# Kernel optimization log

Measured on AMD Instinct MI355X. Metric: run time of the kernel, lower is better.

## Reference

```python
import jax, jax.numpy as jnp
import numpy as np

N_NODES = 100000
N_EDGES = 1600000
N_GRAPH = 100
IN_DIM = 64
LATENT = 128
STEPS = 2
MLP_LAYERS = 2
OUT_GLOBALS = 1
EPS = 1e-5  # haiku LayerNorm default


def setup_inputs() -> dict:
    key = jax.random.key(0)
    ks = jax.random.split(key, 8)
    nodes = jax.random.normal(ks[0], (N_NODES, IN_DIM), jnp.float32)
    senders = jax.random.randint(ks[1], (N_EDGES,), 0, N_NODES, jnp.int32)
    receivers = jax.random.randint(ks[2], (N_EDGES,), 0, N_NODES, jnp.int32)
    # 100 graphs of 1000 nodes each: jnp.repeat(arange(n_graph), n_node)
    graph_ids = (jnp.arange(N_NODES) // (N_NODES // N_GRAPH)).astype(jnp.int32)
    embed_w = jax.random.normal(ks[3], (IN_DIM, LATENT), jnp.float32) / np.sqrt(IN_DIM).astype(np.float32)
    embed_b = jnp.zeros((LATENT,), jnp.float32)
    mlp_w = jax.random.normal(ks[4], (STEPS, MLP_LAYERS, LATENT, LATENT), jnp.float32) / np.sqrt(LATENT).astype(np.float32)
    mlp_b = jnp.zeros((STEPS, MLP_LAYERS, LATENT), jnp.float32)
    ln_scale = jnp.ones((STEPS, LATENT), jnp.float32)
    ln_offset = jnp.zeros((STEPS, LATENT), jnp.float32)
    dec_w = jax.random.normal(ks[5], (LATENT, OUT_GLOBALS), jnp.float32) / np.sqrt(LATENT).astype(np.float32)
    dec_b = jnp.zeros((OUT_GLOBALS,), jnp.float32)
    return dict(nodes=nodes, senders=senders, receivers=receivers, graph_ids=graph_ids,
                embed_w=embed_w, embed_b=embed_b, mlp_w=mlp_w, mlp_b=mlp_b,
                ln_scale=ln_scale, ln_offset=ln_offset, dec_w=dec_w, dec_b=dec_b)


def _layernorm(x, scale, offset):
    mu = jnp.mean(x, axis=-1, keepdims=True)
    var = jnp.var(x, axis=-1, keepdims=True)
    return (x - mu) * jax.lax.rsqrt(var + EPS) * scale + offset


def reference(nodes, senders, receivers, graph_ids, embed_w, embed_b,
              mlp_w, mlp_b, ln_scale, ln_offset, dec_w, dec_b):
    n = nodes.shape[0]
    # jraph.GraphConvolution(add_self_edges=True, symmetric_normalization=True)
    self_loop = jnp.arange(n, dtype=senders.dtype)
    conv_s = jnp.concatenate([senders, self_loop])
    conv_r = jnp.concatenate([receivers, self_loop])
    ones_e = jnp.ones(conv_s.shape[0], jnp.float32)
    inv_sqrt_sdeg = jax.lax.rsqrt(jnp.maximum(jax.ops.segment_sum(ones_e, conv_s, n), 1.0))
    inv_sqrt_rdeg = jax.lax.rsqrt(jnp.maximum(jax.ops.segment_sum(ones_e, conv_r, n), 1.0))

    # embedder: hk.Linear on nodes
    h = nodes @ embed_w + embed_b

    for s in range(STEPS):
        # update_node_fn: MLP (dropout_rate=0 -> identity dropout)
        x = h
        for l in range(MLP_LAYERS):
            x = jax.nn.relu(x @ mlp_w[s, l] + mlp_b[s, l])
        # symmetric-normalized segment_sum aggregation with self-edges
        x = x * inv_sqrt_sdeg[:, None]
        x = jax.ops.segment_sum(x[conv_s], conv_r, num_segments=n)  # [n, LATENT]
        x = x * inv_sqrt_rdeg[:, None]
        h = x + h  # skip connection (add_graphs_tuples)
        h = _layernorm(h, ln_scale[s], ln_offset[s])

    # segment_mean pooling over graphs
    counts = jnp.maximum(jax.ops.segment_sum(jnp.ones(n, jnp.float32), graph_ids, N_GRAPH), 1.0)
    pooled = jax.ops.segment_sum(h, graph_ids, num_segments=N_GRAPH) / counts[:, None]
    # decoder: hk.Linear on pooled globals
    return pooled @ dec_w + dec_b  # [N_GRAPH, OUT_GLOBALS]
```

## Files before the change

### kernel.cpp

```cpp
#include <hip/hip_runtime.h>
#include <hip/hip_bf16.h>


#define N_NODES 100000
#define N_EDGES 1600000
#define N_GRAPH 100
#define NPG     1000
#define LATENT  128

#define NPART   4
#define PSIZE   (N_NODES / NPART)
#define NSLICE  64
#define ESLICE  (N_EDGES / NSLICE)

#define SCAN_CHUNK 2048
#define SCAN_NB    ((N_NODES + SCAN_CHUNK - 1) / SCAN_CHUNK)

typedef __attribute__((ext_vector_type(8))) short short8;
typedef __attribute__((ext_vector_type(4))) float f32x4;

__device__ __forceinline__ unsigned short f2bf(float f) {
    union { float f; unsigned int u; } v; v.f = f;
    unsigned int r = v.u + 0x7fff + ((v.u >> 16) & 1);
    return (unsigned short)(r >> 16);
}
__device__ __forceinline__ float bf2f(unsigned short u) {
    union { unsigned int u; float f; } v; v.u = ((unsigned int)u) << 16;
    return v.f;
}
__device__ __forceinline__ unsigned int pk_fp8x4(float a, float b, float c, float d) {
    int v = 0;
    v = __builtin_amdgcn_cvt_pk_fp8_f32(a, b, v, false);
    v = __builtin_amdgcn_cvt_pk_fp8_f32(c, d, v, true);
    return (unsigned int)v;
}

__global__ __launch_bounds__(1024) void k_hist2(const int* __restrict__ senders,
                                                const int* __restrict__ receivers,
                                                unsigned short* __restrict__ ps16,
                                                unsigned short* __restrict__ pr16) {
    __shared__ unsigned int cs[PSIZE / 2];
    __shared__ unsigned int cr[PSIZE / 2];
    int rg = blockIdx.x & (NPART - 1), sl = blockIdx.x >> 2;
    int lo = rg * PSIZE;
    for (int i = threadIdx.x; i < PSIZE / 2; i += 1024) { cs[i] = 0; cr[i] = 0; }
    __syncthreads();
    int e0 = sl * ESLICE;
    for (int e = e0 + threadIdx.x; e < e0 + ESLICE; e += 1024) {
        int s = senders[e] - lo;
        if ((unsigned)s < PSIZE) atomicAdd(&cs[s >> 1], 1u << ((s & 1) * 16));
        int r = receivers[e] - lo;
        if ((unsigned)r < PSIZE) atomicAdd(&cr[r >> 1], 1u << ((r & 1) * 16));
    }
    __syncthreads();
    size_t base = (size_t)(rg * NSLICE + sl) * PSIZE;
    for (int i = threadIdx.x; i < PSIZE; i += 1024) {
        ps16[base + i] = (unsigned short)((cs[i >> 1] >> ((i & 1) * 16)) & 0xffff);
        pr16[base + i] = (unsigned short)((cr[i >> 1] >> ((i & 1) * 16)) & 0xffff);
    }
}

__global__ __launch_bounds__(256) void k_scan_slices(const unsigned short* __restrict__ ps16,
                                                     unsigned short* __restrict__ pr16,
                                                     int* __restrict__ deg_r,
                                                     float* __restrict__ inv_s,
                                                     float* __restrict__ inv_r,
                                                     int* __restrict__ blocksums) {
    int t = threadIdx.x;
    int n = blockIdx.x * 256 + t;
    int run = 0, ss = 0;
    if (n < N_NODES) {
        int rg = n / PSIZE, i = n - rg * PSIZE;
        size_t base = (size_t)rg * NSLICE * PSIZE + i;
#pragma unroll 4
        for (int sl = 0; sl < NSLICE; sl++) {
            size_t idx = base + (size_t)sl * PSIZE;
            int v = pr16[idx];
            pr16[idx] = (unsigned short)run;
            run += v;
            ss += ps16[idx];
        }
        deg_r[n] = run;
        inv_r[n] = rsqrtf((float)(run + 1));
        inv_s[n] = rsqrtf((float)(ss + 1));
    }
    __shared__ int wsum[4];
    int s = run;
#pragma unroll
    for (int off = 32; off > 0; off >>= 1) s += __shfl_down(s, off, 64);
    if ((t & 63) == 0) wsum[t >> 6] = s;
    __syncthreads();
    if (t == 0)
        atomicAdd(&blocksums[blockIdx.x >> 3], wsum[0] + wsum[1] + wsum[2] + wsum[3]);
}

__global__ __launch_bounds__(256) void k_scan_apply(const int* __restrict__ deg,
                                                    const int* __restrict__ blocksums,
                                                    int* __restrict__ row_start, int n) {
    __shared__ int boff_s;
    int b = blockIdx.x, t = threadIdx.x;
    if (t < 64) {
        int v = (t < b && t < SCAN_NB) ? blocksums[t] : 0;
#pragma unroll
        for (int off = 32; off > 0; off >>= 1) v += __shfl_down(v, off, 64);
        if (t == 0) boff_s = v;
    }
    int base = b * SCAN_CHUNK + t * 8;
    int v[8]; int tsum = 0;
#pragma unroll
    for (int j = 0; j < 8; j++) { int i = base + j; v[j] = (i < n) ? deg[i] : 0; tsum += v[j]; }
    __shared__ int wtot[4];
    int inc = tsum;
#pragma unroll
    for (int off = 1; off < 64; off <<= 1) {
        int u = __shfl_up(inc, off, 64);
        if ((t & 63) >= off) inc += u;
    }
    if ((t & 63) == 63) wtot[t >> 6] = inc;
    __syncthreads();
    int wbase = 0;
    for (int w = 0; w < (t >> 6); w++) wbase += wtot[w];
    int running = boff_s + wbase + (inc - tsum);
#pragma unroll
    for (int j = 0; j < 8; j++) {
        int i = base + j;
        if (i < n) {
            row_start[i] = running;
            running += v[j];
            if (i == n - 1) row_start[n] = running;
        }
    }
}

__global__ __launch_bounds__(1024) void k_fill2(const int* __restrict__ senders,
                                                const int* __restrict__ receivers,
                                                const unsigned short* __restrict__ pr16,
                                                const int* __restrict__ row_start,
                                                int* __restrict__ edge_src) {
    __shared__ int bs[PSIZE];
    int rg = blockIdx.x & (NPART - 1), sl = blockIdx.x >> 2;
    int lo = rg * PSIZE;
    const unsigned short* base = pr16 + (size_t)(rg * NSLICE + sl) * PSIZE;
    for (int i = threadIdx.x; i < PSIZE; i += 1024)
        bs[i] = row_start[lo + i] + (int)base[i];
    __syncthreads();
    int e0 = sl * ESLICE;
    for (int e = e0 + threadIdx.x; e < e0 + ESLICE; e += 1024) {
        int r = receivers[e] - lo;
        if ((unsigned)r < PSIZE) {
            int pos = atomicAdd(&bs[r], 1);
            edge_src[pos] = senders[e];
        }
    }
}

__global__ void k_wprep(const float* __restrict__ embed_w, const float* __restrict__ mlp_w,
                        unsigned short* __restrict__ hi, unsigned short* __restrict__ lo) {
    int t = blockIdx.x * 256 + threadIdx.x;
    if (t >= 8192 + 4 * 16384) return;
    const float* src; int local;
    if (t < 8192) { src = embed_w; local = t; }
    else { int m = t - 8192; src = mlp_w + (size_t)(m >> 14) * 16384; local = m & 16383; }
    int j = local & 7, lane = (local >> 3) & 63, tn = (local >> 9) & 7, kc = local >> 12;
    int k = kc * 32 + ((lane >> 4) << 3) + j;
    int n = tn * 16 + (lane & 15);
    float wv = src[k * 128 + n];
    unsigned short h = f2bf(wv);
    float rem = wv - bf2f(h);
    hi[t] = h; lo[t] = f2bf(rem);
}

__global__ __launch_bounds__(256) void k_embed_mlp(
    const float* __restrict__ A,
    const unsigned short* __restrict__ wehi, const unsigned short* __restrict__ welo,
    const float* __restrict__ eb,
    const unsigned short* __restrict__ w0hi, const unsigned short* __restrict__ w0lo,
    const unsigned short* __restrict__ w1hi, const unsigned short* __restrict__ w1lo,
    const float* __restrict__ b0, const float* __restrict__ b1,
    const float* __restrict__ inv_s,
    unsigned short* __restrict__ h16, unsigned char* __restrict__ x8, int M)
{
    __shared__ __align__(16) unsigned short t0[4][32][136];
    int t = threadIdx.x, w = t >> 6, L = t & 63;
    int m0 = blockIdx.x * 128 + w * 32;
    int lr = L & 15, lk = (L >> 4) * 8, lq = (L >> 4) * 4;

    float ebv[8], b0v[8], b1v[8];
#pragma unroll
    for (int tn = 0; tn < 8; tn++) {
        ebv[tn] = eb[tn * 16 + lr];
        b0v[tn] = b0[tn * 16 + lr];
        b1v[tn] = b1[tn * 16 + lr];
    }

    f32x4 acc[2][8];
#pragma unroll
    for (int bd = 0; bd < 2; bd++)
#pragma unroll
        for (int tn = 0; tn < 8; tn++) acc[bd][tn] = (f32x4){0.f, 0.f, 0.f, 0.f};
#pragma unroll
    for (int kc = 0; kc < 2; kc++) {
        short8 a[2];
#pragma unroll
        for (int bd = 0; bd < 2; bd++) {
            int grow = m0 + bd * 16 + lr; if (grow >= M) grow = M - 1;
            const float* rp = A + (size_t)grow * 64 + kc * 32 + lk;
            float4 v0 = *(const float4*)rp;
            float4 v1 = *(const float4*)(rp + 4);
            short8 pk;
            pk[0] = (short)f2bf(v0.x); pk[1] = (short)f2bf(v0.y);
            pk[2] = (short)f2bf(v0.z); pk[3] = (short)f2bf(v0.w);
            pk[4] = (short)f2bf(v1.x); pk[5] = (short)f2bf(v1.y);
            pk[6] = (short)f2bf(v1.z); pk[7] = (short)f2bf(v1.w);
            a[bd] = pk;
        }
#pragma unroll
        for (int tn = 0; tn < 8; tn++) {
            size_t fo = (size_t)(((kc * 8 + tn) * 64 + L)) * 8;
            short8 bh = *(const short8*)(wehi + fo);
            short8 bl = *(const short8*)(welo + fo);
#pragma unroll
            for (int bd = 0; bd < 2; bd++) {
                acc[bd][tn] = __builtin_amdgcn_mfma_f32_16x16x32_bf16(a[bd], bh, acc[bd][tn], 0, 0, 0);
                acc[bd][tn] = __builtin_amdgcn_mfma_f32_16x16x32_bf16(a[bd], bl, acc[bd][tn], 0, 0, 0);
            }
        }
    }
#pragma unroll
    for (int bd = 0; bd < 2; bd++)
#pragma unroll
        for (int tn = 0; tn < 8; tn++)
#pragma unroll
            for (int r = 0; r < 4; r++)
                t0[w][bd * 16 + lq + r][tn * 16 + lr] = f2bf(acc[bd][tn][r] + ebv[tn]);
#pragma unroll
    for (int q = 0; q < 8; q++) {
        int s = q * 64 + L;
        int row = s >> 4, c0 = (s & 15) * 8;
        int grow = m0 + row;
        if (grow < M)
            *(short8*)(h16 + (size_t)grow * 128 + c0) = *(const short8*)&t0[w][row][c0];
    }

#pragma unroll
    for (int bd = 0; bd < 2; bd++)
#pragma unroll
        for (int tn = 0; tn < 8; tn++) acc[bd][tn] = (f32x4){0.f, 0.f, 0.f, 0.f};
#pragma unroll
    for (int kc = 0; kc < 4; kc++) {
        short8 a[2];
#pragma unroll
        for (int bd = 0; bd < 2; bd++)
            a[bd] = *(const short8*)&t0[w][bd * 16 + lr][kc * 32 + lk];
#pragma unroll
        for (int tn = 0; tn < 8; tn++) {
            size_t fo = (size_t)(((kc * 8 + tn) * 64 + L)) * 8;
            short8 bh = *(const short8*)(w0hi + fo);
            short8 bl = *(const short8*)(w0lo + fo);
#pragma unroll
            for (int bd = 0; bd < 2; bd++) {
                acc[bd][tn] = __builtin_amdgcn_mfma_f32_16x16x32_bf16(a[bd], bh, acc[bd][tn], 0, 0, 0);
                acc[bd][tn] = __builtin_amdgcn_mfma_f32_16x16x32_bf16(a[bd], bl, acc[bd][tn], 0, 0, 0);
            }
        }
    }
#pragma unroll
    for (int bd = 0; bd < 2; bd++)
#pragma unroll
        for (int tn = 0; tn < 8; tn++)
#pragma unroll
            for (int r = 0; r < 4; r++)
                t0[w][bd * 16 + lq + r][tn * 16 + lr] = f2bf(fmaxf(acc[bd][tn][r] + b0v[tn], 0.f));

#pragma unroll
    for (int bd = 0; bd < 2; bd++)
#pragma unroll
        for (int tn = 0; tn < 8; tn++) acc[bd][tn] = (f32x4){0.f, 0.f, 0.f, 0.f};
#pragma unroll
    for (int kc = 0; kc < 4; kc++) {
        short8 a[2];
#pragma unroll
        for (int bd = 0; bd < 2; bd++)
            a[bd] = *(const short8*)&t0[w][bd * 16 + lr][kc * 32 + lk];
#pragma unroll
        for (int tn = 0; tn < 8; tn++) {
            size_t fo = (size_t)(((kc * 8 + tn) * 64 + L)) * 8;
            short8 bh = *(const short8*)(w1hi + fo);
            short8 bl = *(const short8*)(w1lo + fo);
#pragma unroll
            for (int bd = 0; bd < 2; bd++) {
                acc[bd][tn] = __builtin_amdgcn_mfma_f32_16x16x32_bf16(a[bd], bh, acc[bd][tn], 0, 0, 0);
                acc[bd][tn] = __builtin_amdgcn_mfma_f32_16x16x32_bf16(a[bd], bl, acc[bd][tn], 0, 0, 0);
            }
        }
    }
    float invs[2][4];
#pragma unroll
    for (int bd = 0; bd < 2; bd++)
#pragma unroll
        for (int r = 0; r < 4; r++) {
            int grow = m0 + bd * 16 + lq + r; if (grow >= M) grow = M - 1;
            invs[bd][r] = inv_s[grow];
        }
#pragma unroll
    for (int bd = 0; bd < 2; bd++)
#pragma unroll
        for (int tn = 0; tn < 8; tn++)
#pragma unroll
            for (int r = 0; r < 4; r++)
                t0[w][bd * 16 + lq + r][tn * 16 + lr] =
                    f2bf(fmaxf(acc[bd][tn][r] + b1v[tn], 0.f) * invs[bd][r]);
#pragma unroll
    for (int q = 0; q < 8; q++) {
        int s = q * 64 + L;
        int row = s >> 4, c0 = (s & 15) * 8;
        int grow = m0 + row;
        if (grow < M) {
            const unsigned short* sp = &t0[w][row][c0];
            uint2 v;
            v.x = pk_fp8x4(bf2f(sp[0]), bf2f(sp[1]), bf2f(sp[2]), bf2f(sp[3]));
            v.y = pk_fp8x4(bf2f(sp[4]), bf2f(sp[5]), bf2f(sp[6]), bf2f(sp[7]));
            *(uint2*)(x8 + (size_t)grow * 128 + c0) = v;
        }
    }
}

__global__ __launch_bounds__(256) void k_mlp(
    const unsigned short* __restrict__ A16, const unsigned short* __restrict__ w0hi,
    const unsigned short* __restrict__ w0lo, const unsigned short* __restrict__ w1hi,
    const unsigned short* __restrict__ w1lo, const float* __restrict__ b0,
    const float* __restrict__ b1, const float* __restrict__ inv_s,
    unsigned char* __restrict__ x8, int M)
{
    __shared__ __align__(16) unsigned short t1[4][32][136];
    int t = threadIdx.x, w = t >> 6, L = t & 63;
    int m0 = blockIdx.x * 128 + w * 32;
    int lr = L & 15, lk = (L >> 4) * 8, lq = (L >> 4) * 4;

    float b0v[8], b1v[8];
#pragma unroll
    for (int tn = 0; tn < 8; tn++) { b0v[tn] = b0[tn * 16 + lr]; b1v[tn] = b1[tn * 16 + lr]; }

    f32x4 acc[2][8];
#pragma unroll
    for (int bd = 0; bd < 2; bd++)
#pragma unroll
        for (int tn = 0; tn < 8; tn++) acc[bd][tn] = (f32x4){0.f, 0.f, 0.f, 0.f};

#pragma unroll
    for (int kc = 0; kc < 4; kc++) {
        short8 a[2];
#pragma unroll
        for (int bd = 0; bd < 2; bd++) {
            int grow = m0 + bd * 16 + lr; if (grow >= M) grow = M - 1;
            a[bd] = *(const short8*)(A16 + (size_t)grow * 128 + kc * 32 + lk);
        }
#pragma unroll
        for (int tn = 0; tn < 8; tn++) {
            size_t fo = (size_t)(((kc * 8 + tn) * 64 + L)) * 8;
            short8 bh = *(const short8*)(w0hi + fo);
            short8 bl = *(const short8*)(w0lo + fo);
#pragma unroll
            for (int bd = 0; bd < 2; bd++) {
                acc[bd][tn] = __builtin_amdgcn_mfma_f32_16x16x32_bf16(a[bd], bh, acc[bd][tn], 0, 0, 0);
                acc[bd][tn] = __builtin_amdgcn_mfma_f32_16x16x32_bf16(a[bd], bl, acc[bd][tn], 0, 0, 0);
            }
        }
    }
#pragma unroll
    for (int bd = 0; bd < 2; bd++)
#pragma unroll
        for (int tn = 0; tn < 8; tn++)
#pragma unroll
            for (int r = 0; r < 4; r++)
                t1[w][bd * 16 + lq + r][tn * 16 + lr] = f2bf(fmaxf(acc[bd][tn][r] + b0v[tn], 0.f));

    f32x4 acc2[2][8];
#pragma unroll
    for (int bd = 0; bd < 2; bd++)
#pragma unroll
        for (int tn = 0; tn < 8; tn++) acc2[bd][tn] = (f32x4){0.f, 0.f, 0.f, 0.f};
#pragma unroll
    for (int kc = 0; kc < 4; kc++) {
        short8 a[2];
#pragma unroll
        for (int bd = 0; bd < 2; bd++)
            a[bd] = *(const short8*)&t1[w][bd * 16 + lr][kc * 32 + lk];
#pragma unroll
        for (int tn = 0; tn < 8; tn++) {
            size_t fo = (size_t)(((kc * 8 + tn) * 64 + L)) * 8;
            short8 bh = *(const short8*)(w1hi + fo);
            short8 bl = *(const short8*)(w1lo + fo);
#pragma unroll
            for (int bd = 0; bd < 2; bd++) {
                acc2[bd][tn] = __builtin_amdgcn_mfma_f32_16x16x32_bf16(a[bd], bh, acc2[bd][tn], 0, 0, 0);
                acc2[bd][tn] = __builtin_amdgcn_mfma_f32_16x16x32_bf16(a[bd], bl, acc2[bd][tn], 0, 0, 0);
            }
        }
    }
    float invs[2][4];
#pragma unroll
    for (int bd = 0; bd < 2; bd++)
#pragma unroll
        for (int r = 0; r < 4; r++) {
            int grow = m0 + bd * 16 + lq + r; if (grow >= M) grow = M - 1;
            invs[bd][r] = inv_s[grow];
        }
#pragma unroll
    for (int bd = 0; bd < 2; bd++)
#pragma unroll
        for (int tn = 0; tn < 8; tn++)
#pragma unroll
            for (int r = 0; r < 4; r++)
                t1[w][bd * 16 + lq + r][tn * 16 + lr] =
                    f2bf(fmaxf(acc2[bd][tn][r] + b1v[tn], 0.f) * invs[bd][r]);
#pragma unroll
    for (int q = 0; q < 8; q++) {
        int s = q * 64 + L;
        int row = s >> 4, c0 = (s & 15) * 8;
        int grow = m0 + row;
        if (grow < M) {
            const unsigned short* sp = &t1[w][row][c0];
            uint2 v;
            v.x = pk_fp8x4(bf2f(sp[0]), bf2f(sp[1]), bf2f(sp[2]), bf2f(sp[3]));
            v.y = pk_fp8x4(bf2f(sp[4]), bf2f(sp[5]), bf2f(sp[6]), bf2f(sp[7]));
            *(uint2*)(x8 + (size_t)grow * 128 + c0) = v;
        }
    }
}

__device__ __forceinline__ float2 agg_gather8(const unsigned char* __restrict__ x8,
                                              const int* __restrict__ edge_src,
                                              int node, int L, int beg, int end)
{
    unsigned short su = *(const unsigned short*)(x8 + (size_t)node * 128 + 2 * L);
    float2 acc;
    acc.x = __builtin_amdgcn_cvt_f32_fp8((int)su, 0);
    acc.y = __builtin_amdgcn_cvt_f32_fp8((int)su, 1);

    int j = beg;
    for (; j + 8 <= end; j += 8) {
        unsigned short u[8];
#pragma unroll
        for (int q = 0; q < 8; q++)
            u[q] = *(const unsigned short*)(x8 + (size_t)edge_src[j + q] * 128 + 2 * L);
#pragma unroll
        for (int q = 0; q < 8; q++) {
            acc.x += __builtin_amdgcn_cvt_f32_fp8((int)u[q], 0);
            acc.y += __builtin_amdgcn_cvt_f32_fp8((int)u[q], 1);
        }
    }
    if (j < end) {
        int last = end - 1;
        unsigned short u[8];
#pragma unroll
        for (int q = 0; q < 8; q++) {
            int jj = j + q; if (jj > last) jj = last;
            u[q] = *(const unsigned short*)(x8 + (size_t)edge_src[jj] * 128 + 2 * L);
        }
#pragma unroll
        for (int q = 0; q < 8; q++) {
            float a = __builtin_amdgcn_cvt_f32_fp8((int)u[q], 0);
            float b = __builtin_amdgcn_cvt_f32_fp8((int)u[q], 1);
            if (j + q <= last) { acc.x += a; acc.y += b; }
        }
    }
    return acc;
}

__global__ __launch_bounds__(256) void k_agg_ln(
    const unsigned char* __restrict__ x8, const int* __restrict__ row_start,
    const int* __restrict__ edge_src, const float* __restrict__ inv_r,
    const float* __restrict__ ln_scale, const float* __restrict__ ln_offset,
    unsigned short* __restrict__ h16)
{
    int node = __builtin_amdgcn_readfirstlane(blockIdx.x * 4 + (threadIdx.x >> 6));
    int L = threadIdx.x & 63;
    const unsigned int* h32 = (const unsigned int*)h16;

    int beg = row_start[node], end = row_start[node + 1];
    float2 acc = agg_gather8(x8, edge_src, node, L, beg, end);

    float ir = inv_r[node];
    unsigned int hu = h32[(size_t)node * 64 + L];
    float y0 = acc.x * ir + __uint_as_float(hu << 16);
    float y1 = acc.y * ir + __uint_as_float(hu & 0xffff0000u);

    float s1 = y0 + y1, s2 = y0 * y0 + y1 * y1;
#pragma unroll
    for (int off = 32; off > 0; off >>= 1) {
        s1 += __shfl_xor(s1, off, 64);
        s2 += __shfl_xor(s2, off, 64);
    }
    float mu = s1 * (1.f / 128.f);
    float var = fmaxf(s2 * (1.f / 128.f) - mu * mu, 0.f);
    float rstd = rsqrtf(var + 1e-5f);
    float2 sc = *(const float2*)&ln_scale[L * 2];
    float2 of = *(const float2*)&ln_offset[L * 2];
    float ox = (y0 - mu) * rstd * sc.x + of.x;
    float oy = (y1 - mu) * rstd * sc.y + of.y;
    ((unsigned int*)h16)[(size_t)node * 64 + L] =
        (unsigned int)f2bf(ox) | ((unsigned int)f2bf(oy) << 16);
}

__global__ __launch_bounds__(256) void k_agg_pool(
    const unsigned char* __restrict__ x8, const int* __restrict__ row_start,
    const int* __restrict__ edge_src, const float* __restrict__ inv_r,
    const float* __restrict__ ln_scale, const float* __restrict__ ln_offset,
    const unsigned short* __restrict__ h16, float* __restrict__ poolpart)
{
    __shared__ float2 part[4][64];
    int w = threadIdx.x >> 6, L = threadIdx.x & 63;
    int node = __builtin_amdgcn_readfirstlane(blockIdx.x * 4 + w);
    const unsigned int* h32 = (const unsigned int*)h16;

    int beg = row_start[node], end = row_start[node + 1];
    float2 acc = agg_gather8(x8, edge_src, node, L, beg, end);

    float ir = inv_r[node];
    unsigned int hu = h32[(size_t)node * 64 + L];
    float y0 = acc.x * ir + __uint_as_float(hu << 16);
    float y1 = acc.y * ir + __uint_as_float(hu & 0xffff0000u);

    float s1 = y0 + y1, s2 = y0 * y0 + y1 * y1;
#pragma unroll
    for (int off = 32; off > 0; off >>= 1) {
        s1 += __shfl_xor(s1, off, 64);
        s2 += __shfl_xor(s2, off, 64);
    }
    float mu = s1 * (1.f / 128.f);
    float var = fmaxf(s2 * (1.f / 128.f) - mu * mu, 0.f);
    float rstd = rsqrtf(var + 1e-5f);
    float2 sc = *(const float2*)&ln_scale[L * 2];
    float2 of = *(const float2*)&ln_offset[L * 2];
    float2 o;
    o.x = (y0 - mu) * rstd * sc.x + of.x;
    o.y = (y1 - mu) * rstd * sc.y + of.y;
    part[w][L] = o;
    __syncthreads();
    if (w == 0) {
        float2 p0 = part[0][L], p1 = part[1][L], p2 = part[2][L], p3 = part[3][L];
        float2 s;
        s.x = (p0.x + p1.x) + (p2.x + p3.x);
        s.y = (p0.y + p1.y) + (p2.y + p3.y);
        *(float2*)&poolpart[(size_t)blockIdx.x * 128 + L * 2] = s;
    }
}

__global__ __launch_bounds__(128) void k_pool2(const float* __restrict__ poolpart,
                                               float* __restrict__ poolpart2) {
    int b = blockIdx.x, col = threadIdx.x;
    const float* pg = poolpart + ((size_t)b * 25) * 128;
    float s = 0.f;
#pragma unroll
    for (int k = 0; k < 25; k++) s += pg[k * 128 + col];
    poolpart2[(size_t)b * 128 + col] = s;
}

__global__ __launch_bounds__(128) void k_pool3(const float* __restrict__ poolpart2,
                                               const float* __restrict__ dec_w,
                                               const float* __restrict__ dec_b,
                                               float* __restrict__ out) {
    int g = blockIdx.x, col = threadIdx.x;
    const float* pg = poolpart2 + (size_t)g * 10 * 128;
    float s = 0.f;
#pragma unroll
    for (int c = 0; c < 10; c++) s += pg[c * 128 + col];
    s = s * (1.f / (float)NPG) * dec_w[col];
    __shared__ float ws[2];
#pragma unroll
    for (int off = 32; off > 0; off >>= 1) s += __shfl_down(s, off, 64);
    if ((col & 63) == 0) ws[col >> 6] = s;
    __syncthreads();
    if (col == 0) out[g] = ws[0] + ws[1] + dec_b[0];
}

extern "C" void kernel_launch(void* const* d_in, const int* in_sizes, int n_in,
                              void* d_out, int out_size, void* d_ws, size_t ws_size,
                              hipStream_t stream) {
    (void)in_sizes; (void)n_in; (void)out_size; (void)ws_size;
    const float* nodes     = (const float*)d_in[0];
    const int*   senders   = (const int*)d_in[1];
    const int*   receivers = (const int*)d_in[2];
    const float* embed_w   = (const float*)d_in[4];
    const float* embed_b   = (const float*)d_in[5];
    const float* mlp_w     = (const float*)d_in[6];
    const float* mlp_b     = (const float*)d_in[7];
    const float* ln_scale  = (const float*)d_in[8];
    const float* ln_offset = (const float*)d_in[9];
    const float* dec_w     = (const float*)d_in[10];
    const float* dec_b     = (const float*)d_in[11];
    float* out = (float*)d_out;

    const int N = N_NODES;
    const int WF_TOTAL = 8192 + 4 * 16384;
    const size_t PART_TOTAL = (size_t)NPART * NSLICE * PSIZE;

    char* p = (char*)d_ws;
    auto alloc = [&](size_t bytes) -> void* {
        void* r = (void*)p;
        p += (bytes + 255) & ~(size_t)255;
        return r;
    };
    unsigned short* h16      = (unsigned short*)alloc((size_t)N * 128 * 2);
    unsigned char*  x8       = (unsigned char*)alloc((size_t)N * 128);
    int*            edge_src = (int*)alloc((size_t)N_EDGES * 4);
    unsigned short* ps16     = (unsigned short*)alloc(PART_TOTAL * 2);
    unsigned short* pr16     = (unsigned short*)alloc(PART_TOTAL * 2);
    int*            deg_r    = (int*)alloc((size_t)N * 4);
    float*          inv_s    = (float*)alloc((size_t)N * 4);
    float*          inv_r    = (float*)alloc((size_t)N * 4);
    int*            row_start= (int*)alloc((size_t)(N + 1) * 4);
    int*            blocksums= (int*)alloc((size_t)SCAN_NB * 4);
    unsigned short* wfhi     = (unsigned short*)alloc((size_t)WF_TOTAL * 2);
    unsigned short* wflo     = (unsigned short*)alloc((size_t)WF_TOTAL * 2);
    float*          poolpart = (float*)alloc((size_t)(N / 4) * 128 * 4);
    float*          poolpart2= (float*)alloc((size_t)1000 * 128 * 4);

    hipMemsetAsync(blocksums, 0, (size_t)SCAN_NB * 4, stream);
    k_wprep<<<(WF_TOTAL + 255) / 256, 256, 0, stream>>>(embed_w, mlp_w, wfhi, wflo);

    k_hist2<<<NPART * NSLICE, 1024, 0, stream>>>(senders, receivers, ps16, pr16);
    k_scan_slices<<<(N + 255) / 256, 256, 0, stream>>>(ps16, pr16, deg_r, inv_s, inv_r, blocksums);
    k_scan_apply<<<SCAN_NB, 256, 0, stream>>>(deg_r, blocksums, row_start, N);
    k_fill2<<<NPART * NSLICE, 1024, 0, stream>>>(senders, receivers, pr16, row_start, edge_src);

    int mblocks = (N + 127) / 128;
    const unsigned short* wehi = wfhi, *welo = wflo;
    const unsigned short* w0hi[2] = { wfhi + 8192,             wfhi + 8192 + 2 * 16384 };
    const unsigned short* w0lo[2] = { wflo + 8192,             wflo + 8192 + 2 * 16384 };
    const unsigned short* w1hi[2] = { wfhi + 8192 + 16384,     wfhi + 8192 + 3 * 16384 };
    const unsigned short* w1lo[2] = { wflo + 8192 + 16384,     wflo + 8192 + 3 * 16384 };

    k_embed_mlp<<<mblocks, 256, 0, stream>>>(nodes, wehi, welo, embed_b,
                                             w0hi[0], w0lo[0], w1hi[0], w1lo[0],
                                             mlp_b, mlp_b + 128, inv_s, h16, x8, N);
    k_agg_ln<<<N / 4, 256, 0, stream>>>(x8, row_start, edge_src, inv_r,
                                        ln_scale, ln_offset, h16);
    k_mlp<<<mblocks, 256, 0, stream>>>(h16, w0hi[1], w0lo[1], w1hi[1], w1lo[1],
                                       mlp_b + 256, mlp_b + 384, inv_s, x8, N);
    k_agg_pool<<<N / 4, 256, 0, stream>>>(x8, row_start, edge_src, inv_r,
                                          ln_scale + 128, ln_offset + 128, h16, poolpart);

    k_pool2<<<1000, 128, 0, stream>>>(poolpart, poolpart2);
    k_pool3<<<N_GRAPH, 128, 0, stream>>>(poolpart2, dec_w, dec_b, out);
}
```

Baseline: 355.2 us.

## Record per-edge rank in histogram pass and fill CSR without atomics

Measured after the change: 366.7 us. +3.2%, slower.

```diff
diff --git a/kernel.cpp b/kernel.cpp
--- a/kernel.cpp
+++ b/kernel.cpp
@@ -38,7 +38,8 @@
 __global__ __launch_bounds__(1024) void k_hist2(const int* __restrict__ senders,
                                                 const int* __restrict__ receivers,
                                                 unsigned short* __restrict__ ps16,
-                                                unsigned short* __restrict__ pr16) {
+                                                unsigned short* __restrict__ pr16,
+                                                unsigned short* __restrict__ rank) {
     __shared__ unsigned int cs[PSIZE / 2];
     __shared__ unsigned int cr[PSIZE / 2];
     int rg = blockIdx.x & (NPART - 1), sl = blockIdx.x >> 2;
@@ -50,7 +51,10 @@
         int s = senders[e] - lo;
         if ((unsigned)s < PSIZE) atomicAdd(&cs[s >> 1], 1u << ((s & 1) * 16));
         int r = receivers[e] - lo;
-        if ((unsigned)r < PSIZE) atomicAdd(&cr[r >> 1], 1u << ((r & 1) * 16));
+        if ((unsigned)r < PSIZE) {
+            unsigned int old = atomicAdd(&cr[r >> 1], 1u << ((r & 1) * 16));
+            rank[e] = (unsigned short)((old >> ((r & 1) * 16)) & 0xffff);
+        }
     }
     __syncthreads();
     size_t base = (size_t)(rg * NSLICE + sl) * PSIZE;
@@ -132,26 +136,20 @@
     }
 }
 
-__global__ __launch_bounds__(1024) void k_fill2(const int* __restrict__ senders,
-                                                const int* __restrict__ receivers,
-                                                const unsigned short* __restrict__ pr16,
-                                                const int* __restrict__ row_start,
-                                                int* __restrict__ edge_src) {
-    __shared__ int bs[PSIZE];
-    int rg = blockIdx.x & (NPART - 1), sl = blockIdx.x >> 2;
-    int lo = rg * PSIZE;
-    const unsigned short* base = pr16 + (size_t)(rg * NSLICE + sl) * PSIZE;
-    for (int i = threadIdx.x; i < PSIZE; i += 1024)
-        bs[i] = row_start[lo + i] + (int)base[i];
-    __syncthreads();
-    int e0 = sl * ESLICE;
-    for (int e = e0 + threadIdx.x; e < e0 + ESLICE; e += 1024) {
-        int r = receivers[e] - lo;
-        if ((unsigned)r < PSIZE) {
-            int pos = atomicAdd(&bs[r], 1);
-            edge_src[pos] = senders[e];
-        }
-    }
+__global__ __launch_bounds__(256) void k_fill3(const int* __restrict__ senders,
+                                               const int* __restrict__ receivers,
+                                               const unsigned short* __restrict__ rank,
+                                               const unsigned short* __restrict__ pr16,
+                                               const int* __restrict__ row_start,
+                                               int* __restrict__ edge_src) {
+    int e = blockIdx.x * 256 + threadIdx.x;
+    if (e >= N_EDGES) return;
+    int r = receivers[e];
+    int sl = e / ESLICE;
+    int rg = r / PSIZE;
+    int i = r - rg * PSIZE;
+    int off = pr16[(size_t)(rg * NSLICE + sl) * PSIZE + i];
+    edge_src[row_start[r] + off + (int)rank[e]] = senders[e];
 }
 
 __global__ void k_wprep(const float* __restrict__ embed_w, const float* __restrict__ mlp_w,
@@ -605,6 +603,7 @@
     unsigned short* h16      = (unsigned short*)alloc((size_t)N * 128 * 2);
     unsigned char*  x8       = (unsigned char*)alloc((size_t)N * 128);
     int*            edge_src = (int*)alloc((size_t)N_EDGES * 4);
+    unsigned short* rank     = (unsigned short*)alloc((size_t)N_EDGES * 2);
     unsigned short* ps16     = (unsigned short*)alloc(PART_TOTAL * 2);
     unsigned short* pr16     = (unsigned short*)alloc(PART_TOTAL * 2);
     int*            deg_r    = (int*)alloc((size_t)N * 4);
@@ -620,10 +619,11 @@
     hipMemsetAsync(blocksums, 0, (size_t)SCAN_NB * 4, stream);
     k_wprep<<<(WF_TOTAL + 255) / 256, 256, 0, stream>>>(embed_w, mlp_w, wfhi, wflo);
 
-    k_hist2<<<NPART * NSLICE, 1024, 0, stream>>>(senders, receivers, ps16, pr16);
+    k_hist2<<<NPART * NSLICE, 1024, 0, stream>>>(senders, receivers, ps16, pr16, rank);
     k_scan_slices<<<(N + 255) / 256, 256, 0, stream>>>(ps16, pr16, deg_r, inv_s, inv_r, blocksums);
     k_scan_apply<<<SCAN_NB, 256, 0, stream>>>(deg_r, blocksums, row_start, N);
-    k_fill2<<<NPART * NSLICE, 1024, 0, stream>>>(senders, receivers, pr16, row_start, edge_src);
+    k_fill3<<<(N_EDGES + 255) / 256, 256, 0, stream>>>(senders, receivers, rank, pr16,
+                                                       row_start, edge_src);
 
     int mblocks = (N + 127) / 128;
     const unsigned short* wehi = wfhi, *welo = wflo;
```
